# Performance work log

Hardware: AMD Instinct MI355X
Metric: run time of the kernel (lower is better)

The kernel has to match this reference:

```python
import jax, jax.numpy as jnp
import numpy as np

N_NODES = 50000
N_EDGES = 800000
D = 128
VOCAB = 50000


def setup_inputs() -> dict:
    key = jax.random.key(0)
    k1, k2, k3, k4, k5 = jax.random.split(key, 5)
    feat = jax.random.randint(k1, (N_NODES,), 0, VOCAB, dtype=jnp.int64 if jax.config.jax_enable_x64 else jnp.int32).astype(jnp.int32)
    src = jax.random.randint(k2, (N_EDGES,), 0, N_NODES, dtype=jnp.int32)
    dst = jax.random.randint(k3, (N_EDGES,), 0, N_NODES, dtype=jnp.int32)
    embedding = jax.random.normal(k4, (VOCAB, D), dtype=jnp.float32)
    bias_param = jax.random.normal(k5, (D,), dtype=jnp.float32)
    return {"feat": feat, "src": src, "dst": dst, "embedding": embedding, "bias_param": bias_param}


def reference(feat, src, dst, embedding, bias_param):
    n = feat.shape[0]
    ones = jnp.ones(src.shape[0], dtype=jnp.float32)
    # out-degree (per source node) left normalization, norm='both' -> deg^{-1/2}
    out_deg = jax.ops.segment_sum(ones, src, num_segments=n)
    norm_l = jnp.power(jnp.clip(out_deg, 1.0, None), -0.5)
    h = embedding[feat] * norm_l[:, None]          # [N, D]
    msg = h[src]                                    # [E, D] gather
    rst = jax.ops.segment_sum(msg, dst, num_segments=n)  # [N, D] scatter-sum
    # in-degree right normalization
    in_deg = jax.ops.segment_sum(ones, dst, num_segments=n)
    norm_r = jnp.power(jnp.clip(in_deg, 1.0, None), -0.5)
    rst = rst * norm_r[:, None] + bias_param
    return rst
```

## Files before the change

kernel.cpp:

```cpp
#include <hip/hip_runtime.h>

#define NN 50000
#define NE 800000
#define DD 128
#define BSH 6
#define BSZ 64
#define NBUCK ((NN + BSZ - 1) / BSZ)
#define NBLK 256
#define EPB ((NE + NBLK - 1) / NBLK)

__device__ __forceinline__ unsigned short f2bf(float x) {
    unsigned u = __float_as_uint(x);
    unsigned r = u + 0x7FFF + ((u >> 16) & 1);
    return (unsigned short)(r >> 16);
}
__device__ __forceinline__ float bf2f(unsigned short x) {
    return __uint_as_float((unsigned)x << 16);
}

__global__ void hist_kernel(const int* __restrict__ src, const int* __restrict__ dst,
                            int* __restrict__ histD, int* __restrict__ histS) {
    __shared__ int hD[NBUCK], hS[NBUCK];
    int t = threadIdx.x, blk = blockIdx.x;
    for (int b = t; b < NBUCK; b += 256) { hD[b] = 0; hS[b] = 0; }
    __syncthreads();
    int beg = blk * EPB, end = min(beg + EPB, NE);
    for (int i = beg + t; i < end; i += 256) {
        atomicAdd(&hD[dst[i] >> BSH], 1);
        atomicAdd(&hS[src[i] >> BSH], 1);
    }
    __syncthreads();
    for (int b = t; b < NBUCK; b += 256) {
        histD[b * NBLK + blk] = hD[b];
        histS[b * NBLK + blk] = hS[b];
    }
}

__global__ void within_kernel(int* __restrict__ histD, int* __restrict__ histS,
                              int* __restrict__ SD, int* __restrict__ SS) {
    __shared__ int col[NBLK];
    int t = threadIdx.x, b = blockIdx.x;
    int* hist = (b < NBUCK) ? histD : histS;
    int* S = (b < NBUCK) ? SD : SS;
    int bin = (b < NBUCK) ? b : b - NBUCK;
    int v = hist[bin * NBLK + t];
    col[t] = v;
    __syncthreads();
    for (int off = 1; off < NBLK; off <<= 1) {
        int x = (t >= off) ? col[t - off] : 0;
        __syncthreads();
        col[t] += x;
        __syncthreads();
    }
    hist[bin * NBLK + t] = col[t] - v;
    if (t == NBLK - 1) S[bin] = col[t];
}

__global__ void scan_kernel(const int* __restrict__ SD, const int* __restrict__ SS,
                            int* __restrict__ baseD, int* __restrict__ baseS) {
    __shared__ int s[1024];
    int t = threadIdx.x;
    for (int pass = 0; pass < 2; pass++) {
        const int* S = pass ? SS : SD;
        int* base = pass ? baseS : baseD;
        int v = (t < NBUCK) ? S[t] : 0;
        s[t] = v;
        __syncthreads();
        for (int off = 1; off < 1024; off <<= 1) {
            int x = (t >= off) ? s[t - off] : 0;
            __syncthreads();
            s[t] += x;
            __syncthreads();
        }
        if (t < NBUCK) base[t] = s[t] - v;
        __syncthreads();
    }
}

__global__ void scatter_kernel(const int* __restrict__ src, const int* __restrict__ dst,
                               const int* __restrict__ offsD, const int* __restrict__ offsS,
                               const int* __restrict__ baseD, const int* __restrict__ baseS,
                               unsigned int* __restrict__ sortedD,
                               unsigned char* __restrict__ sortedS) {
    __shared__ int curD[NBUCK], curS[NBUCK];
    int t = threadIdx.x, blk = blockIdx.x;
    for (int b = t; b < NBUCK; b += 256) {
        curD[b] = baseD[b] + offsD[b * NBLK + blk];
        curS[b] = baseS[b] + offsS[b * NBLK + blk];
    }
    __syncthreads();
    int beg = blk * EPB, end = min(beg + EPB, NE);
    for (int i = beg + t; i < end; i += 256) {
        int sv = src[i], dv = dst[i];
        int pD = atomicAdd(&curD[dv >> BSH], 1);
        sortedD[pD] = (unsigned)sv | ((unsigned)(dv & (BSZ - 1)) << 16);
        int pS = atomicAdd(&curS[sv >> BSH], 1);
        sortedS[pS] = (unsigned char)(sv & (BSZ - 1));
    }
}

__global__ void finehb_kernel(const unsigned int* __restrict__ sortedD,
                              const unsigned char* __restrict__ sortedS,
                              const int* __restrict__ baseD, const int* __restrict__ baseS,
                              const int* __restrict__ feat, const float* __restrict__ emb,
                              int* __restrict__ baseN, int* __restrict__ cntN,
                              unsigned short* __restrict__ srcfine,
                              ushort4* __restrict__ h4) {
    __shared__ int lh[BSZ], lcur[BSZ];
    int t = threadIdx.x;
    if (blockIdx.x < NBUCK) {
        int bin = blockIdx.x;
        int beg = baseD[bin];
        int end = (bin == NBUCK - 1) ? NE : baseD[bin + 1];
        if (t < BSZ) lh[t] = 0;
        __syncthreads();
        for (int i = beg + t; i < end; i += 256) atomicAdd(&lh[sortedD[i] >> 16], 1);
        __syncthreads();
        if (t < BSZ) {
            int v = lh[t];
            int x = v;
            for (int off = 1; off < 64; off <<= 1) {
                int y = __shfl_up(x, off);
                if (t >= off) x += y;
            }
            int excl = beg + x - v;
            lcur[t] = excl;
            int n = (bin << BSH) + t;
            if (n < NN) { baseN[n] = excl; cntN[n] = v; }
        }
        __syncthreads();
        for (int i = beg + t; i < end; i += 256) {
            unsigned e = sortedD[i];
            int pos = atomicAdd(&lcur[e >> 16], 1);
            srcfine[pos] = (unsigned short)(e & 0xFFFF);
        }
    } else {
        int bin = blockIdx.x - NBUCK;
        int beg = baseS[bin];
        int end = (bin == NBUCK - 1) ? NE : baseS[bin + 1];
        if (t < BSZ) lh[t] = 0;
        __syncthreads();
        for (int i = beg + t; i < end; i += 256) atomicAdd(&lh[sortedS[i]], 1);
        __syncthreads();
        int w = t >> 6, lane = t & 63;
        int half = lane >> 5, sl = lane & 31;
        for (int k = 0; k < 8; k++) {
            int lo = (w << 4) + (k << 1) + half;
            int n = (bin << BSH) + lo;
            if (n < NN) {
                float nl = rsqrtf((float)max(lh[lo], 1));
                int f = feat[n];
                float4 v = ((const float4*)(emb + (size_t)f * DD))[sl];
                h4[(size_t)n * 32 + sl] =
                    make_ushort4(f2bf(v.x * nl), f2bf(v.y * nl), f2bf(v.z * nl), f2bf(v.w * nl));
            }
        }
    }
}

__global__ void gatherA_kernel(const unsigned short* __restrict__ srcfine,
                               const int* __restrict__ baseN, const int* __restrict__ cntN,
                               const ushort4* __restrict__ h4, const float* __restrict__ bias,
                               float* __restrict__ out) {
    int wid = (blockIdx.x * blockDim.x + threadIdx.x) >> 6;
    int lane = threadIdx.x & 63;
    if (wid >= NN) return;
    int half = lane >> 5, sl = lane & 31;
    int cnt = cntN[wid];
    int beg = baseN[wid];
    float a0 = 0.f, a1 = 0.f, a2 = 0.f, a3 = 0.f;
    for (int b0 = 0; b0 < cnt; b0 += 64) {
        int m = min(cnt - b0, 64);
        int idx = (lane < m) ? (int)srcfine[beg + b0 + lane] : 0;
        int j = 0;
        for (; j + 7 < m; j += 8) {
            int s0 = __shfl(idx, j + half);
            int s1 = __shfl(idx, j + 2 + half);
            int s2 = __shfl(idx, j + 4 + half);
            int s3 = __shfl(idx, j + 6 + half);
            ushort4 v0 = h4[(size_t)s0 * 32 + sl];
            ushort4 v1 = h4[(size_t)s1 * 32 + sl];
            ushort4 v2 = h4[(size_t)s2 * 32 + sl];
            ushort4 v3 = h4[(size_t)s3 * 32 + sl];
            a0 += bf2f(v0.x) + bf2f(v1.x) + bf2f(v2.x) + bf2f(v3.x);
            a1 += bf2f(v0.y) + bf2f(v1.y) + bf2f(v2.y) + bf2f(v3.y);
            a2 += bf2f(v0.z) + bf2f(v1.z) + bf2f(v2.z) + bf2f(v3.z);
            a3 += bf2f(v0.w) + bf2f(v1.w) + bf2f(v2.w) + bf2f(v3.w);
        }
        for (; j + 1 < m; j += 2) {
            int s0 = __shfl(idx, j + half);
            ushort4 v0 = h4[(size_t)s0 * 32 + sl];
            a0 += bf2f(v0.x);
            a1 += bf2f(v0.y);
            a2 += bf2f(v0.z);
            a3 += bf2f(v0.w);
        }
        if (j < m) {
            int s0 = __shfl(idx, j);
            if (half == 0) {
                ushort4 v0 = h4[(size_t)s0 * 32 + sl];
                a0 += bf2f(v0.x);
                a1 += bf2f(v0.y);
                a2 += bf2f(v0.z);
                a3 += bf2f(v0.w);
            }
        }
    }
    a0 += __shfl_xor(a0, 32);
    a1 += __shfl_xor(a1, 32);
    a2 += __shfl_xor(a2, 32);
    a3 += __shfl_xor(a3, 32);
    if (half == 0) {
        float nr = rsqrtf((float)max(cnt, 1));
        float4 bi = ((const float4*)bias)[sl];
        ((float4*)(out + (size_t)wid * DD))[sl] =
            make_float4(a0 * nr + bi.x, a1 * nr + bi.y, a2 * nr + bi.z, a3 * nr + bi.w);
    }
}

extern "C" void kernel_launch(void* const* d_in, const int* in_sizes, int n_in,
                              void* d_out, int out_size, void* d_ws, size_t ws_size,
                              hipStream_t stream) {
    const int* feat = (const int*)d_in[0];
    const int* src  = (const int*)d_in[1];
    const int* dst  = (const int*)d_in[2];
    const float* emb  = (const float*)d_in[3];
    const float* bias = (const float*)d_in[4];
    float* out = (float*)d_out;

    int* histD = (int*)d_ws;
    int* histS = histD + NBUCK * NBLK;
    int* SD    = histS + NBUCK * NBLK;
    int* SS    = SD + 800;
    int* baseD = SS + 800;
    int* baseS = baseD + 800;
    int* baseN = baseS + 800;
    int* cntN  = baseN + NN;
    unsigned int* sortedD = (unsigned int*)(cntN + NN);
    ushort4* h4 = (ushort4*)(sortedD + NE);
    unsigned short* srcfine = (unsigned short*)(h4 + (size_t)NN * 32);
    unsigned char* sortedS = (unsigned char*)(srcfine + NE);

    hist_kernel<<<NBLK, 256, 0, stream>>>(src, dst, histD, histS);
    within_kernel<<<2 * NBUCK, NBLK, 0, stream>>>(histD, histS, SD, SS);
    scan_kernel<<<1, 1024, 0, stream>>>(SD, SS, baseD, baseS);
    scatter_kernel<<<NBLK, 256, 0, stream>>>(src, dst, histD, histS, baseD, baseS,
                                             sortedD, sortedS);
    finehb_kernel<<<2 * NBUCK, 256, 0, stream>>>(sortedD, sortedS, baseD, baseS, feat, emb,
                                                 baseN, cntN, srcfine, h4);
    gatherA_kernel<<<(NN * 64 + 255) / 256, 256, 0, stream>>>(srcfine, baseN, cntN, h4, bias, out);
}
```

Baseline: 83.25 us.

## Double partition blocks and fold bucket scan into scatter kernel

Doubles the number of edge-partition blocks in the histogram and scatter passes from 256 to 512. The within-bucket scan now handles two entries per thread. The separate single-block bucket-prefix scan kernel is removed: each scatter block recomputes the 782-entry bucket scan redundantly, and block 0 writes the base arrays. This saves one launch and uses more CUs for the atomic-heavy passes, at the cost of redundant scan work in every scatter block and larger histogram arrays.

After: 85.49 us. 1.03x slower.

```diff
diff --git a/kernel.cpp b/kernel.cpp
--- a/kernel.cpp
+++ b/kernel.cpp
@@ -6,8 +6,9 @@
 #define BSH 6
 #define BSZ 64
 #define NBUCK ((NN + BSZ - 1) / BSZ)
-#define NBLK 256
-#define EPB ((NE + NBLK - 1) / NBLK)
+#define NBLKP 512
+#define EPB ((NE + NBLKP - 1) / NBLKP)
+#define TPB 256
 
 __device__ __forceinline__ unsigned short f2bf(float x) {
     unsigned u = __float_as_uint(x);
@@ -22,75 +23,106 @@
                             int* __restrict__ histD, int* __restrict__ histS) {
     __shared__ int hD[NBUCK], hS[NBUCK];
     int t = threadIdx.x, blk = blockIdx.x;
-    for (int b = t; b < NBUCK; b += 256) { hD[b] = 0; hS[b] = 0; }
+    for (int b = t; b < NBUCK; b += TPB) { hD[b] = 0; hS[b] = 0; }
     __syncthreads();
     int beg = blk * EPB, end = min(beg + EPB, NE);
-    for (int i = beg + t; i < end; i += 256) {
+    for (int i = beg + t; i < end; i += TPB) {
         atomicAdd(&hD[dst[i] >> BSH], 1);
         atomicAdd(&hS[src[i] >> BSH], 1);
     }
     __syncthreads();
-    for (int b = t; b < NBUCK; b += 256) {
-        histD[b * NBLK + blk] = hD[b];
-        histS[b * NBLK + blk] = hS[b];
+    for (int b = t; b < NBUCK; b += TPB) {
+        histD[b * NBLKP + blk] = hD[b];
+        histS[b * NBLKP + blk] = hS[b];
     }
 }
 
 __global__ void within_kernel(int* __restrict__ histD, int* __restrict__ histS,
                               int* __restrict__ SD, int* __restrict__ SS) {
-    __shared__ int col[NBLK];
+    __shared__ int col[TPB];
     int t = threadIdx.x, b = blockIdx.x;
     int* hist = (b < NBUCK) ? histD : histS;
     int* S = (b < NBUCK) ? SD : SS;
     int bin = (b < NBUCK) ? b : b - NBUCK;
-    int v = hist[bin * NBLK + t];
-    col[t] = v;
-    __syncthreads();
-    for (int off = 1; off < NBLK; off <<= 1) {
+    int2 e = ((int2*)(hist + (size_t)bin * NBLKP))[t];
+    int s = e.x + e.y;
+    col[t] = s;
+    __syncthreads();
+    for (int off = 1; off < TPB; off <<= 1) {
         int x = (t >= off) ? col[t - off] : 0;
         __syncthreads();
         col[t] += x;
         __syncthreads();
     }
-    hist[bin * NBLK + t] = col[t] - v;
-    if (t == NBLK - 1) S[bin] = col[t];
-}
-
-__global__ void scan_kernel(const int* __restrict__ SD, const int* __restrict__ SS,
-                            int* __restrict__ baseD, int* __restrict__ baseS) {
-    __shared__ int s[1024];
-    int t = threadIdx.x;
-    for (int pass = 0; pass < 2; pass++) {
-        const int* S = pass ? SS : SD;
-        int* base = pass ? baseS : baseD;
-        int v = (t < NBUCK) ? S[t] : 0;
-        s[t] = v;
-        __syncthreads();
-        for (int off = 1; off < 1024; off <<= 1) {
-            int x = (t >= off) ? s[t - off] : 0;
-            __syncthreads();
-            s[t] += x;
-            __syncthreads();
-        }
-        if (t < NBUCK) base[t] = s[t] - v;
-        __syncthreads();
-    }
+    int excl = col[t] - s;
+    ((int2*)(hist + (size_t)bin * NBLKP))[t] = make_int2(excl, excl + e.x);
+    if (t == TPB - 1) S[bin] = excl + s;
 }
 
 __global__ void scatter_kernel(const int* __restrict__ src, const int* __restrict__ dst,
                                const int* __restrict__ offsD, const int* __restrict__ offsS,
-                               const int* __restrict__ baseD, const int* __restrict__ baseS,
+                               const int* __restrict__ SD, const int* __restrict__ SS,
+                               int* __restrict__ baseD, int* __restrict__ baseS,
                                unsigned int* __restrict__ sortedD,
                                unsigned char* __restrict__ sortedS) {
-    __shared__ int curD[NBUCK], curS[NBUCK];
+    __shared__ int curD[NBUCK], curS[NBUCK], scr[TPB];
     int t = threadIdx.x, blk = blockIdx.x;
-    for (int b = t; b < NBUCK; b += 256) {
-        curD[b] = baseD[b] + offsD[b * NBLK + blk];
-        curS[b] = baseS[b] + offsS[b * NBLK + blk];
+    {
+        int e[4], s = 0;
+        for (int k = 0; k < 4; k++) {
+            int i = 4 * t + k;
+            e[k] = (i < NBUCK) ? SD[i] : 0;
+            s += e[k];
+        }
+        scr[t] = s;
+        __syncthreads();
+        for (int off = 1; off < TPB; off <<= 1) {
+            int x = (t >= off) ? scr[t - off] : 0;
+            __syncthreads();
+            scr[t] += x;
+            __syncthreads();
+        }
+        int excl = scr[t] - s;
+        for (int k = 0; k < 4; k++) {
+            int i = 4 * t + k;
+            if (i < NBUCK) curD[i] = excl;
+            excl += e[k];
+        }
+    }
+    __syncthreads();
+    {
+        int e[4], s = 0;
+        for (int k = 0; k < 4; k++) {
+            int i = 4 * t + k;
+            e[k] = (i < NBUCK) ? SS[i] : 0;
+            s += e[k];
+        }
+        scr[t] = s;
+        __syncthreads();
+        for (int off = 1; off < TPB; off <<= 1) {
+            int x = (t >= off) ? scr[t - off] : 0;
+            __syncthreads();
+            scr[t] += x;
+            __syncthreads();
+        }
+        int excl = scr[t] - s;
+        for (int k = 0; k < 4; k++) {
+            int i = 4 * t + k;
+            if (i < NBUCK) curS[i] = excl;
+            excl += e[k];
+        }
+    }
+    __syncthreads();
+    if (blk == 0) {
+        for (int b = t; b < NBUCK; b += TPB) { baseD[b] = curD[b]; baseS[b] = curS[b]; }
+    }
+    for (int b = t; b < NBUCK; b += TPB) {
+        curD[b] += offsD[b * NBLKP + blk];
+        curS[b] += offsS[b * NBLKP + blk];
     }
     __syncthreads();
     int beg = blk * EPB, end = min(beg + EPB, NE);
-    for (int i = beg + t; i < end; i += 256) {
+    for (int i = beg + t; i < end; i += TPB) {
         int sv = src[i], dv = dst[i];
         int pD = atomicAdd(&curD[dv >> BSH], 1);
         sortedD[pD] = (unsigned)sv | ((unsigned)(dv & (BSZ - 1)) << 16);
@@ -114,7 +146,7 @@
         int end = (bin == NBUCK - 1) ? NE : baseD[bin + 1];
         if (t < BSZ) lh[t] = 0;
         __syncthreads();
-        for (int i = beg + t; i < end; i += 256) atomicAdd(&lh[sortedD[i] >> 16], 1);
+        for (int i = beg + t; i < end; i += TPB) atomicAdd(&lh[sortedD[i] >> 16], 1);
         __syncthreads();
         if (t < BSZ) {
             int v = lh[t];
@@ -129,7 +161,7 @@
             if (n < NN) { baseN[n] = excl; cntN[n] = v; }
         }
         __syncthreads();
-        for (int i = beg + t; i < end; i += 256) {
+        for (int i = beg + t; i < end; i += TPB) {
             unsigned e = sortedD[i];
             int pos = atomicAdd(&lcur[e >> 16], 1);
             srcfine[pos] = (unsigned short)(e & 0xFFFF);
@@ -140,7 +172,7 @@
         int end = (bin == NBUCK - 1) ? NE : baseS[bin + 1];
         if (t < BSZ) lh[t] = 0;
         __syncthreads();
-        for (int i = beg + t; i < end; i += 256) atomicAdd(&lh[sortedS[i]], 1);
+        for (int i = beg + t; i < end; i += TPB) atomicAdd(&lh[sortedS[i]], 1);
         __syncthreads();
         int w = t >> 6, lane = t & 63;
         int half = lane >> 5, sl = lane & 31;
@@ -229,8 +261,8 @@
     float* out = (float*)d_out;
 
     int* histD = (int*)d_ws;
-    int* histS = histD + NBUCK * NBLK;
-    int* SD    = histS + NBUCK * NBLK;
+    int* histS = histD + (size_t)NBUCK * NBLKP;
+    int* SD    = histS + (size_t)NBUCK * NBLKP;
     int* SS    = SD + 800;
     int* baseD = SS + 800;
     int* baseS = baseD + 800;
@@ -241,12 +273,12 @@
     unsigned short* srcfine = (unsigned short*)(h4 + (size_t)NN * 32);
     unsigned char* sortedS = (unsigned char*)(srcfine + NE);
 
-    hist_kernel<<<NBLK, 256, 0, stream>>>(src, dst, histD, histS);
-    within_kernel<<<2 * NBUCK, NBLK, 0, stream>>>(histD, histS, SD, SS);
-    scan_kernel<<<1, 1024, 0, stream>>>(SD, SS, baseD, baseS);
-    scatter_kernel<<<NBLK, 256, 0, stream>>>(src, dst, histD, histS, baseD, baseS,
-                                             sortedD, sortedS);
-    finehb_kernel<<<2 * NBUCK, 256, 0, stream>>>(sortedD, sortedS, baseD, baseS, feat, emb,
+    hist_kernel<<<NBLKP, TPB, 0, stream>>>(src, dst, histD, histS);
+    within_kernel<<<2 * NBUCK, TPB, 0, stream>>>(histD, histS, SD, SS);
+    scatter_kernel<<<NBLKP, TPB, 0, stream>>>(src, dst, histD, histS, SD, SS,
+                                              baseD, baseS, sortedD, sortedS);
+    finehb_kernel<<<2 * NBUCK, TPB, 0, stream>>>(sortedD, sortedS, baseD, baseS, feat, emb,
                                                  baseN, cntN, srcfine, h4);
-    gatherA_kernel<<<(NN * 64 + 255) / 256, 256, 0, stream>>>(srcfine, baseN, cntN, h4, bias, out);
-}
+    gatherA_kernel<<<(NN * 64 + TPB - 1) / TPB, TPB, 0, stream>>>(srcfine, baseN, cntN,
+                                                                  h4, bias, out);
+}
```
